# Kernel tuning notes

Measured on AMD Instinct MI355X. Metric: run time of the kernel, lower is better.

The kernel has to match this reference:

```python
import jax, jax.numpy as jnp
import numpy as np

BATCH, NUM_TREE, TOTAL_NODES, WIDTH = 256, 64, 341, 4  # depth=4 -> 1024 leaves


def setup_inputs() -> dict:
    key = jax.random.key(0)
    inputs = jax.random.normal(key, (BATCH, NUM_TREE, TOTAL_NODES, WIDTH), dtype=jnp.float32)
    return {"inputs": inputs}


def reference(inputs):
    """Soft decision forest: per-node softmax over `width` branches, leaf prob =
    product of branch probs along the root->leaf path. Node indices follow the
    original DFS preorder; leaves are emitted in DFS order.
    Input: [B, T, total_nodes, width] -> Output: [B, T, width**(depth+1)].
    """
    B, T, N, W = inputs.shape
    # invert total_nodes = sum_{z=0}^{depth} W^z  (same formula as _depth_calc)
    depth = int(round(np.log(1 - N * (1 - W)) / np.log(W) - 1))
    D = depth + 1  # number of internal levels traversed (call uses depth+1)

    P = jax.nn.softmax(inputs, axis=-1)  # [B, T, N, W]

    w = jnp.ones((B, T, 1), dtype=inputs.dtype)  # leaf-prefix weights
    idx = np.zeros(1, dtype=np.int64)            # DFS node indices for current level
    for l in range(D):
        probs = jnp.take(P, jnp.asarray(idx), axis=2)      # [B, T, K, W]
        w = (w[..., None] * probs).reshape(B, T, -1)        # [B, T, K*W]
        # child j of preorder node i with (D-l-1) remaining levels below child:
        # child_idx = i + 1 + j * s(D-l-1), s(m) = (W^m - 1)/(W - 1)
        s_child = (W ** (D - 1 - l) - 1) // (W - 1)
        idx = (idx[:, None] + 1 + np.arange(W, dtype=np.int64) * s_child).reshape(-1)
    return w  # [B, T, W**D]
```

## Files before the change

kernel.cpp:

```cpp
#include <hip/hip_runtime.h>


#define NUM_NODES 341

__global__ __launch_bounds__(256) void forest_kernel(const float* __restrict__ in,
                                                     float* __restrict__ out) {
    __shared__ float4 sP[4][NUM_NODES];

    const int tid  = threadIdx.x;
    const int wave = tid >> 6;
    const int lane = tid & 63;
    const int bt   = blockIdx.x * 4 + wave;

    float4* sPw = sP[wave];
    const float* sPf = reinterpret_cast<const float*>(sPw);

    const float4* in4 = reinterpret_cast<const float4*>(in) + (size_t)bt * NUM_NODES;
    float4 v[6];
#pragma unroll
    for (int i = 0; i < 5; ++i) v[i] = in4[lane + 64 * i];
    const bool tail = (lane < NUM_NODES - 320);
    if (tail) v[5] = in4[lane + 320];

#pragma unroll
    for (int i = 0; i < 6; ++i) {
        if (i < 5 || tail) {
            float4 x = v[i];
            float m  = fmaxf(fmaxf(x.x, x.y), fmaxf(x.z, x.w));
            float e0 = __expf(x.x - m);
            float e1 = __expf(x.y - m);
            float e2 = __expf(x.z - m);
            float e3 = __expf(x.w - m);
            float r  = 1.0f / (e0 + e1 + e2 + e3);
            sPw[lane + 64 * i] = make_float4(e0 * r, e1 * r, e2 * r, e3 * r);
        }
    }

    asm volatile("s_waitcnt lgkmcnt(0)" ::: "memory");
    __builtin_amdgcn_sched_barrier(0);

    const int j1 = lane >> 4;
    const int j2 = (lane >> 2) & 3;
    const int j3 = lane & 3;

    float4* out4 = reinterpret_cast<float4*>(out) + (size_t)bt * 256;

#pragma unroll
    for (int j0 = 0; j0 < 4; ++j0) {
        const int n1 = 1 + 85 * j0;
        const int n2 = n1 + 1 + 21 * j1;
        const int n3 = n2 + 1 + 5 * j2;
        const int n4 = n3 + 1 + j3;

        const float pre = sPf[j0]
                        * sPf[n1 * 4 + j1]
                        * sPf[n2 * 4 + j2]
                        * sPf[n3 * 4 + j3];

        float4 pv = sPw[n4];
        out4[j0 * 64 + lane] = make_float4(pre * pv.x, pre * pv.y,
                                           pre * pv.z, pre * pv.w);
    }
}

extern "C" void kernel_launch(void* const* d_in, const int* in_sizes, int n_in,
                              void* d_out, int out_size, void* d_ws, size_t ws_size,
                              hipStream_t stream) {
    const float* in = (const float*)d_in[0];
    float* out = (float*)d_out;
    const int num_blocks = (256 * 64) / 4;
    forest_kernel<<<num_blocks, 256, 0, stream>>>(in, out);
}
```

Baseline: 28.62 us.

## Drop LDS staging; load path nodes directly and recompute softmax per lane

```diff
diff --git a/kernel.cpp b/kernel.cpp
--- a/kernel.cpp
+++ b/kernel.cpp
@@ -3,61 +3,60 @@
 
 #define NUM_NODES 341
 
+__device__ __forceinline__ float4 softmax4(float4 x) {
+    float m  = fmaxf(fmaxf(x.x, x.y), fmaxf(x.z, x.w));
+    float e0 = __expf(x.x - m);
+    float e1 = __expf(x.y - m);
+    float e2 = __expf(x.z - m);
+    float e3 = __expf(x.w - m);
+    float r  = 1.0f / (e0 + e1 + e2 + e3);
+    return make_float4(e0 * r, e1 * r, e2 * r, e3 * r);
+}
+
+__device__ __forceinline__ float selc(float4 v, int c) {
+    float ab = (c & 1) ? v.y : v.x;
+    float cd = (c & 1) ? v.w : v.z;
+    return (c & 2) ? cd : ab;
+}
+
 __global__ __launch_bounds__(256) void forest_kernel(const float* __restrict__ in,
                                                      float* __restrict__ out) {
-    __shared__ float4 sP[4][NUM_NODES];
-
     const int tid  = threadIdx.x;
     const int wave = tid >> 6;
     const int lane = tid & 63;
     const int bt   = blockIdx.x * 4 + wave;
 
-    float4* sPw = sP[wave];
-    const float* sPf = reinterpret_cast<const float*>(sPw);
-
-    const float4* in4 = reinterpret_cast<const float4*>(in) + (size_t)bt * NUM_NODES;
-    float4 v[6];
-#pragma unroll
-    for (int i = 0; i < 5; ++i) v[i] = in4[lane + 64 * i];
-    const bool tail = (lane < NUM_NODES - 320);
-    if (tail) v[5] = in4[lane + 320];
-
-#pragma unroll
-    for (int i = 0; i < 6; ++i) {
-        if (i < 5 || tail) {
-            float4 x = v[i];
-            float m  = fmaxf(fmaxf(x.x, x.y), fmaxf(x.z, x.w));
-            float e0 = __expf(x.x - m);
-            float e1 = __expf(x.y - m);
-            float e2 = __expf(x.z - m);
-            float e3 = __expf(x.w - m);
-            float r  = 1.0f / (e0 + e1 + e2 + e3);
-            sPw[lane + 64 * i] = make_float4(e0 * r, e1 * r, e2 * r, e3 * r);
-        }
-    }
-
-    asm volatile("s_waitcnt lgkmcnt(0)" ::: "memory");
-    __builtin_amdgcn_sched_barrier(0);
+    const float4* base = reinterpret_cast<const float4*>(in) + (size_t)bt * NUM_NODES;
 
     const int j1 = lane >> 4;
     const int j2 = (lane >> 2) & 3;
     const int j3 = lane & 3;
 
-    float4* out4 = reinterpret_cast<float4*>(out) + (size_t)bt * 256;
-
+    float4 r0 = base[0];
+    float4 r1[4], r2[4], r3[4], r4[4];
 #pragma unroll
     for (int j0 = 0; j0 < 4; ++j0) {
         const int n1 = 1 + 85 * j0;
         const int n2 = n1 + 1 + 21 * j1;
         const int n3 = n2 + 1 + 5 * j2;
         const int n4 = n3 + 1 + j3;
+        r1[j0] = base[n1];
+        r2[j0] = base[n2];
+        r3[j0] = base[n3];
+        r4[j0] = base[n4];
+    }
 
-        const float pre = sPf[j0]
-                        * sPf[n1 * 4 + j1]
-                        * sPf[n2 * 4 + j2]
-                        * sPf[n3 * 4 + j3];
+    const float4 p0 = softmax4(r0);
 
-        float4 pv = sPw[n4];
+    float4* out4 = reinterpret_cast<float4*>(out) + (size_t)bt * 256;
+
+#pragma unroll
+    for (int j0 = 0; j0 < 4; ++j0) {
+        const float pre = selc(p0, j0)
+                        * selc(softmax4(r1[j0]), j1)
+                        * selc(softmax4(r2[j0]), j2)
+                        * selc(softmax4(r3[j0]), j3);
+        const float4 pv = softmax4(r4[j0]);
         out4[j0 * 64 + lane] = make_float4(pre * pv.x, pre * pv.y,
                                            pre * pv.z, pre * pv.w);
     }
```

Result: slower. 30.96 us (+8.2%).
